# Kernel tuning notes

Measured on AMD Instinct MI355X. Metric: run time of the kernel, lower is better.

The kernel has to match this reference:

```python
import jax, jax.numpy as jnp
import numpy as np
import math

B, L, H, NH = 4, 1024, 512, 8
D = H // NH

def setup_inputs() -> dict:
    key = jax.random.key(0)
    ks = jax.random.split(key, 12)
    s = 1.0 / math.sqrt(H)
    return {
        "key": jax.random.normal(ks[0], (B, L, H), jnp.float32),
        "query": jax.random.normal(ks[1], (B, L, H), jnp.float32),
        "value": jax.random.normal(ks[2], (B, L, H), jnp.float32),
        "rel_pos_embedding": jax.random.normal(ks[3], (B, NH, L, L), jnp.float32),
        "wk_w": jax.random.normal(ks[4], (H, H), jnp.float32) * s,
        "wk_b": jnp.zeros((H,), jnp.float32),
        "wq_w": jax.random.normal(ks[5], (H, H), jnp.float32) * s,
        "wq_b": jnp.zeros((H,), jnp.float32),
        "wv_w": jax.random.normal(ks[6], (H, H), jnp.float32) * s,
        "wv_b": jnp.zeros((H,), jnp.float32),
        "ff_w": jax.random.normal(ks[7], (H, H), jnp.float32) * s,
        "ff_b": jnp.zeros((H,), jnp.float32),
        "seq_len": jax.random.randint(ks[8], (B,), 1, 768, jnp.int32),
        "lex_num": jax.random.randint(ks[9], (B,), 0, 256, jnp.int32),
    }

def reference(key, query, value, rel_pos_embedding, wk_w, wk_b, wq_w, wq_b, wv_w, wv_b, ff_w, ff_b, seq_len, lex_num):
    b, l, h = key.shape
    # projections (torch Linear: x @ W^T + b)
    k = (key @ wk_w.T + wk_b).reshape(b, l, NH, D)
    q = (query @ wq_w.T + wq_b).reshape(b, l, NH, D)
    v = (value @ wv_w.T + wv_b).reshape(b, l, NH, D)
    # QK^T: [b, nh, lq, lk]
    scores = jnp.einsum("bqhd,bkhd->bhqk", q, k) / math.sqrt(D)
    scores = scores + rel_pos_embedding
    # padding mask over key positions
    lengths = (seq_len + lex_num).astype(jnp.int32)  # [b]
    mask = jnp.arange(l, dtype=jnp.int32)[None, :] < lengths[:, None]  # [b, l]
    scores = jnp.where(mask[:, None, None, :], scores, jnp.float32(-1e15))
    attn = jax.nn.softmax(scores, axis=-1)
    out = jnp.einsum("bhqk,bkhd->bqhd", attn, v).reshape(b, l, h)
    out = out @ ff_w.T + ff_b
    return out
```

## Files before the change

### kernel.cpp

```cpp
#include <hip/hip_runtime.h>
#include <hip/hip_bf16.h>

typedef __attribute__((ext_vector_type(8))) short bf16x8;
typedef __attribute__((ext_vector_type(4))) float f32x4;

__device__ __forceinline__ unsigned short f2bf(float f) {
    return __builtin_bit_cast(unsigned short, __float2bfloat16(f));
}

typedef const __attribute__((address_space(1))) void gvoid;
typedef __attribute__((address_space(3))) void lvoid;
#define GLDS(g, s) __builtin_amdgcn_global_load_lds((gvoid*)(g), (lvoid*)(s), 16, 0, 0)

__device__ __forceinline__ void block_barrier() {
    asm volatile("" ::: "memory");
    __builtin_amdgcn_s_barrier();
    asm volatile("" ::: "memory");
}

__global__ __launch_bounds__(256) void proj_kernel(
    const float* __restrict__ query, const float* __restrict__ key_, const float* __restrict__ value,
    const float* __restrict__ wq_w, const float* __restrict__ wq_b,
    const float* __restrict__ wk_w, const float* __restrict__ wk_b,
    const float* __restrict__ wv_w, const float* __restrict__ wv_b,
    unsigned short* __restrict__ Qb, unsigned short* __restrict__ Kb, unsigned short* __restrict__ Vt)
{
    const int wid = (blockIdx.x & 7) * 48 + (blockIdx.x >> 3);
    const int z = wid >> 7;
    const int rr = wid & 127;
    const int by = rr >> 2, bx = rr & 3;

    const float* X    = (z == 0) ? query : (z == 1) ? key_ : value;
    const float* W    = (z == 0) ? wq_w  : (z == 1) ? wk_w : wv_w;
    const float* bias = (z == 0) ? wq_b  : (z == 1) ? wk_b : wv_b;

    const int t = threadIdx.x;
    const int l = t & 63;
    const int w = t >> 6;
    const int wm = w >> 1, wn = w & 1;
    const int m0 = by * 128, n0 = bx * 128;

    __shared__ __align__(16) unsigned short As[128 * 32];
    __shared__ __align__(16) unsigned short Bs[128 * 32];

    f32x4 acc[4][4];
#pragma unroll
    for (int i = 0; i < 4; i++)
#pragma unroll
        for (int j = 0; j < 4; j++) acc[i][j] = (f32x4){0.f, 0.f, 0.f, 0.f};

    float4 ra[4], rb[4];
    auto LOAD = [&](int k0) {
#pragma unroll
        for (int i = 0; i < 4; i++) {
            int idx = t + 256 * i;
            int row = idx >> 3, c = idx & 7;
            ra[i] = *(const float4*)(X + (size_t)(m0 + row) * 512 + k0 + c * 4);
            rb[i] = *(const float4*)(W + (size_t)(n0 + row) * 512 + k0 + c * 4);
        }
    };
    LOAD(0);

    for (int k0 = 0; k0 < 512; k0 += 32) {
        if (k0) block_barrier();
#pragma unroll
        for (int i = 0; i < 4; i++) {
            int idx = t + 256 * i;
            int row = idx >> 3, c = idx & 7;
            __align__(8) unsigned short va[4] = {f2bf(ra[i].x), f2bf(ra[i].y), f2bf(ra[i].z), f2bf(ra[i].w)};
            *(uint2*)(As + row * 32 + (((c >> 1) ^ (row & 3)) * 8) + (c & 1) * 4) = *(uint2*)va;
            __align__(8) unsigned short vb[4] = {f2bf(rb[i].x), f2bf(rb[i].y), f2bf(rb[i].z), f2bf(rb[i].w)};
            *(uint2*)(Bs + row * 32 + (((c >> 1) ^ (row & 3)) * 8) + (c & 1) * 4) = *(uint2*)vb;
        }
        asm volatile("s_waitcnt lgkmcnt(0)" ::: "memory");
        block_barrier();
        if (k0 + 32 < 512) LOAD(k0 + 32);

        bf16x8 af[4], bfv[4];
#pragma unroll
        for (int mf = 0; mf < 4; mf++) {
            int row = wm * 64 + mf * 16 + (l & 15);
            af[mf] = *(const bf16x8*)(As + row * 32 + (((l >> 4) ^ (row & 3)) * 8));
        }
#pragma unroll
        for (int nf = 0; nf < 4; nf++) {
            int row = wn * 64 + nf * 16 + (l & 15);
            bfv[nf] = *(const bf16x8*)(Bs + row * 32 + (((l >> 4) ^ (row & 3)) * 8));
        }
#pragma unroll
        for (int mf = 0; mf < 4; mf++)
#pragma unroll
            for (int nf = 0; nf < 4; nf++)
                acc[mf][nf] = __builtin_amdgcn_mfma_f32_16x16x32_bf16(af[mf], bfv[nf], acc[mf][nf], 0, 0, 0);
    }

    if (z < 2) {
        unsigned short* dst = (z == 0) ? Qb : Kb;
#pragma unroll
        for (int nf = 0; nf < 4; nf++) {
            int n = n0 + wn * 64 + nf * 16 + (l & 15);
            float bv = bias[n];
            int h = n >> 6, d = n & 63;
#pragma unroll
            for (int mf = 0; mf < 4; mf++) {
                int mbase = m0 + wm * 64 + mf * 16 + 4 * (l >> 4);
                int bb = mbase >> 10;
#pragma unroll
                for (int r = 0; r < 4; r++) {
                    int lq = (mbase + r) & 1023;
                    dst[((size_t)(bb * 8 + h) * 1024 + lq) * 64 + d] = f2bf(acc[mf][nf][r] + bv);
                }
            }
        }
    } else {
#pragma unroll
        for (int nf = 0; nf < 4; nf++) {
            int n = n0 + wn * 64 + nf * 16 + (l & 15);
            float bv = bias[n];
            int h = n >> 6, d = n & 63;
#pragma unroll
            for (int mf = 0; mf < 4; mf++) {
                int mbase = m0 + wm * 64 + mf * 16 + 4 * (l >> 4);
                int bb = mbase >> 10;
                int lq0 = mbase & 1023;
                ushort4 pk;
                pk.x = f2bf(acc[mf][nf][0] + bv);
                pk.y = f2bf(acc[mf][nf][1] + bv);
                pk.z = f2bf(acc[mf][nf][2] + bv);
                pk.w = f2bf(acc[mf][nf][3] + bv);
                *(ushort4*)(Vt + ((size_t)(bb * 8 + h) * 64 + d) * 1024 + lq0) = pk;
            }
        }
    }
}

__global__ __launch_bounds__(256, 3) void attn_kernel(
    const unsigned short* __restrict__ Qb, const unsigned short* __restrict__ Kb,
    const unsigned short* __restrict__ Vt, const float* __restrict__ rel_pos,
    const int* __restrict__ seq_len, const int* __restrict__ lex_num,
    unsigned short* __restrict__ AO)
{
    const int t = threadIdx.x;
    const int l = t & 63;
    const int w = t >> 6;
    const int wid = (blockIdx.x & 7) * 64 + (blockIdx.x >> 3);
    const int x8 = wid >> 6;
    const int g  = (wid >> 4) & 3;
    const int qt = wid & 15;
    const int b  = g;
    const int h  = (x8 + 2 * g) & 7;
    const int q0 = qt * 64;
    const int bh = b * 8 + h;
    const int len = seq_len[b] + lex_num[b];
    const int nkt = (len + 63) >> 6;

    __shared__ __align__(16) unsigned short Qs[64 * 64];
    __shared__ __align__(16) unsigned short Ks[2][64 * 64];
    __shared__ __align__(16) unsigned short Vs[2][64 * 64];
    __shared__ __align__(16) unsigned short Ps[4 * 16 * 64];

    const unsigned short* Qg = Qb + ((size_t)bh * 1024 + q0) * 64;
    const unsigned short* Kg = Kb + (size_t)bh * 1024 * 64;
    const unsigned short* Vg = Vt + (size_t)bh * 64 * 1024;
    const float* Rg = rel_pos + ((size_t)bh * 1024 + q0) * 1024;

    const int rl8 = l >> 3, c8 = l & 7;
    const int kvc = (c8 ^ rl8) * 8;

    auto STAGE_KV = [&](int kt2, int nb) {
        const int k0s = kt2 * 64;
#pragma unroll
        for (int j = 0; j < 2; j++) {
            int row = w * 16 + j * 8 + rl8;
            GLDS(Kg + (size_t)(k0s + row) * 64 + kvc, &Ks[nb][(w * 16 + j * 8) * 64]);
            GLDS(Vg + (size_t)row * 1024 + k0s + kvc, &Vs[nb][(w * 16 + j * 8) * 64]);
        }
    };
    auto RELLOAD = [&](float (&R)[16], int kt2) {
        const float* rp = Rg + (size_t)(w * 16 + 4 * (l >> 4)) * 1024 + kt2 * 64 + (l & 15);
#pragma unroll
        for (int r = 0; r < 4; r++)
#pragma unroll
            for (int kn = 0; kn < 4; kn++)
                R[4 * r + kn] = rp[(size_t)r * 1024 + kn * 16];
    };

    float rA[16], rB[16];
#pragma unroll
    for (int j = 0; j < 2; j++) {
        int row = w * 16 + j * 8 + rl8;
        GLDS(Qg + (size_t)row * 64 + kvc, &Qs[(w * 16 + j * 8) * 64]);
    }
    STAGE_KV(0, 0);
    RELLOAD(rA, 0);

    bf16x8 qf[2];
    f32x4 oacc[4];
#pragma unroll
    for (int dn = 0; dn < 4; dn++) oacc[dn] = (f32x4){0.f, 0.f, 0.f, 0.f};
    float m_run[4] = {-3.0e38f, -3.0e38f, -3.0e38f, -3.0e38f};
    float l_run[4] = {0.f, 0.f, 0.f, 0.f};
    unsigned short* Pw = Ps + w * 1024;

    auto tile_body = [&](int kt, float (&REL)[16], float (&RELN)[16]) {
        const int cur = kt & 1;
        const int k0 = kt * 64;
        if (kt + 1 < nkt) {
            STAGE_KV(kt + 1, cur ^ 1);
            RELLOAD(RELN, kt + 1);
            asm volatile("s_waitcnt vmcnt(20)" ::: "memory");
        } else {
            asm volatile("s_waitcnt vmcnt(0)" ::: "memory");
        }
        block_barrier();

        if (kt == 0) {
#pragma unroll
            for (int s = 0; s < 2; s++) {
                int row = w * 16 + (l & 15);
                int ch = 4 * s + (l >> 4);
                qf[s] = *(const bf16x8*)(Qs + row * 64 + ((ch ^ (row & 7)) * 8));
            }
        }

        const unsigned short* Ksc = Ks[cur];
        const unsigned short* Vsc = Vs[cur];

        f32x4 sa[4];
#pragma unroll
        for (int kn = 0; kn < 4; kn++) sa[kn] = (f32x4){0.f, 0.f, 0.f, 0.f};
        __builtin_amdgcn_s_setprio(1);
#pragma unroll
        for (int s = 0; s < 2; s++)
#pragma unroll
            for (int kn = 0; kn < 4; kn++) {
                int krow = kn * 16 + (l & 15);
                int ch = 4 * s + (l >> 4);
                bf16x8 kf = *(const bf16x8*)(Ksc + krow * 64 + ((ch ^ (krow & 7)) * 8));
                sa[kn] = __builtin_amdgcn_mfma_f32_16x16x32_bf16(qf[s], kf, sa[kn], 0, 0, 0);
            }
        __builtin_amdgcn_s_setprio(0);

        float p[4][4];
#pragma unroll
        for (int r = 0; r < 4; r++) {
            float sv[4];
#pragma unroll
            for (int kn = 0; kn < 4; kn++) {
                int kg = k0 + kn * 16 + (l & 15);
                float x = sa[kn][r] * 0.125f + REL[4 * r + kn];
                sv[kn] = (kg < len) ? x : -1e15f;
            }
            float mx = fmaxf(fmaxf(sv[0], sv[1]), fmaxf(sv[2], sv[3]));
#pragma unroll
            for (int o = 1; o < 16; o <<= 1) mx = fmaxf(mx, __shfl_xor(mx, o, 64));
            float mn = fmaxf(m_run[r], mx);
            float scale = __expf(m_run[r] - mn);
            m_run[r] = mn;
            float rs = 0.f;
#pragma unroll
            for (int kn = 0; kn < 4; kn++) { p[kn][r] = __expf(sv[kn] - mn); rs += p[kn][r]; }
#pragma unroll
            for (int o = 1; o < 16; o <<= 1) rs += __shfl_xor(rs, o, 64);
            l_run[r] = l_run[r] * scale + rs;
#pragma unroll
            for (int dn = 0; dn < 4; dn++) oacc[dn][r] *= scale;
        }

#pragma unroll
        for (int kn = 0; kn < 4; kn++)
#pragma unroll
            for (int r = 0; r < 4; r++) {
                int qrow = 4 * (l >> 4) + r;
                int k = kn * 16 + (l & 15);
                Pw[qrow * 64 + (((k >> 3) ^ (qrow & 7)) * 8) + (k & 7)] = f2bf(p[kn][r]);
            }

        __builtin_amdgcn_s_setprio(1);
#pragma unroll
        for (int s = 0; s < 2; s++) {
            int arow = (l & 15);
            bf16x8 pf = *(const bf16x8*)(Pw + arow * 64 + (((4 * s + (l >> 4)) ^ (arow & 7)) * 8));
#pragma unroll
            for (int dn = 0; dn < 4; dn++) {
                int drow = dn * 16 + (l & 15);
                bf16x8 vf = *(const bf16x8*)(Vsc + drow * 64 + (((4 * s + (l >> 4)) ^ (drow & 7)) * 8));
                oacc[dn] = __builtin_amdgcn_mfma_f32_16x16x32_bf16(pf, vf, oacc[dn], 0, 0, 0);
            }
        }
        __builtin_amdgcn_s_setprio(0);
        block_barrier();
    };

    for (int kt = 0; kt < nkt; kt += 2) {
        tile_body(kt, rA, rB);
        if (kt + 1 < nkt) tile_body(kt + 1, rB, rA);
    }

    unsigned short* AOg = AO + ((size_t)(b * 1024 + q0 + w * 16)) * 512 + h * 64;
#pragma unroll
    for (int r = 0; r < 4; r++) {
        float inv = 1.0f / l_run[r];
        int qrow = 4 * (l >> 4) + r;
#pragma unroll
        for (int dn = 0; dn < 4; dn++)
            AOg[(size_t)qrow * 512 + dn * 16 + (l & 15)] = f2bf(oacc[dn][r] * inv);
    }
}

__global__ __launch_bounds__(256) void ff_kernel(
    const unsigned short* __restrict__ AO, const float* __restrict__ ff_w,
    const float* __restrict__ ff_b, float* __restrict__ out)
{
    const int t = threadIdx.x;
    const int l = t & 63;
    const int w = t >> 6;
    const int wm = w >> 1, wn = w & 1;
    const int wid = (blockIdx.x & 7) * 32 + (blockIdx.x >> 3);
    const int by = wid >> 2;
    const int bx = wid & 3;
    const int m0 = by * 64, n0 = bx * 128;

    __shared__ __align__(16) unsigned short As[64 * 32];
    __shared__ __align__(16) unsigned short Bs[128 * 32];

    f32x4 acc[2][4];
#pragma unroll
    for (int i = 0; i < 2; i++)
#pragma unroll
        for (int j = 0; j < 4; j++) acc[i][j] = (f32x4){0.f, 0.f, 0.f, 0.f};

    uint4 ua;
    float4 rbf[4];
    const int arow = t >> 2, ac = t & 3;
    auto LOAD = [&](int k0) {
        ua = *(const uint4*)(AO + (size_t)(m0 + arow) * 512 + k0 + ac * 8);
#pragma unroll
        for (int i = 0; i < 4; i++) {
            int idx = t + 256 * i;
            int row = idx >> 3, c = idx & 7;
            rbf[i] = *(const float4*)(ff_w + (size_t)(n0 + row) * 512 + k0 + c * 4);
        }
    };
    LOAD(0);

    for (int k0 = 0; k0 < 512; k0 += 32) {
        if (k0) block_barrier();
        *(uint4*)(As + arow * 32 + ((ac ^ (arow & 3)) * 8)) = ua;
#pragma unroll
        for (int i = 0; i < 4; i++) {
            int idx = t + 256 * i;
            int row = idx >> 3, c = idx & 7;
            __align__(8) unsigned short vb[4] = {f2bf(rbf[i].x), f2bf(rbf[i].y), f2bf(rbf[i].z), f2bf(rbf[i].w)};
            *(uint2*)(Bs + row * 32 + (((c >> 1) ^ (row & 3)) * 8) + (c & 1) * 4) = *(uint2*)vb;
        }
        asm volatile("s_waitcnt lgkmcnt(0)" ::: "memory");
        block_barrier();
        if (k0 + 32 < 512) LOAD(k0 + 32);

        bf16x8 af[2], bfv[4];
#pragma unroll
        for (int mf = 0; mf < 2; mf++) {
            int row = wm * 32 + mf * 16 + (l & 15);
            af[mf] = *(const bf16x8*)(As + row * 32 + (((l >> 4) ^ (row & 3)) * 8));
        }
#pragma unroll
        for (int nf = 0; nf < 4; nf++) {
            int row = wn * 64 + nf * 16 + (l & 15);
            bfv[nf] = *(const bf16x8*)(Bs + row * 32 + (((l >> 4) ^ (row & 3)) * 8));
        }
#pragma unroll
        for (int mf = 0; mf < 2; mf++)
#pragma unroll
            for (int nf = 0; nf < 4; nf++)
                acc[mf][nf] = __builtin_amdgcn_mfma_f32_16x16x32_bf16(af[mf], bfv[nf], acc[mf][nf], 0, 0, 0);
    }

#pragma unroll
    for (int nf = 0; nf < 4; nf++) {
        int n = n0 + wn * 64 + nf * 16 + (l & 15);
        float bv = ff_b[n];
#pragma unroll
        for (int mf = 0; mf < 2; mf++) {
            int mbase = m0 + wm * 32 + mf * 16 + 4 * (l >> 4);
#pragma unroll
            for (int r = 0; r < 4; r++)
                out[(size_t)(mbase + r) * 512 + n] = acc[mf][nf][r] + bv;
        }
    }
}

extern "C" void kernel_launch(void* const* d_in, const int* in_sizes, int n_in,
                              void* d_out, int out_size, void* d_ws, size_t ws_size,
                              hipStream_t stream) {
    const float* key   = (const float*)d_in[0];
    const float* query = (const float*)d_in[1];
    const float* value = (const float*)d_in[2];
    const float* rel   = (const float*)d_in[3];
    const float* wk_w  = (const float*)d_in[4];
    const float* wk_b  = (const float*)d_in[5];
    const float* wq_w  = (const float*)d_in[6];
    const float* wq_b  = (const float*)d_in[7];
    const float* wv_w  = (const float*)d_in[8];
    const float* wv_b  = (const float*)d_in[9];
    const float* ff_w  = (const float*)d_in[10];
    const float* ff_b  = (const float*)d_in[11];
    const int* seq_len = (const int*)d_in[12];
    const int* lex_num = (const int*)d_in[13];
    float* out = (float*)d_out;

    unsigned short* Qb = (unsigned short*)d_ws;
    unsigned short* Kb = Qb + 2097152;
    unsigned short* Vt = Kb + 2097152;
    unsigned short* AO = Vt + 2097152;

    proj_kernel<<<dim3(384), 256, 0, stream>>>(query, key, value,
                                               wq_w, wq_b, wk_w, wk_b, wv_w, wv_b,
                                               Qb, Kb, Vt);
    attn_kernel<<<dim3(512), 256, 0, stream>>>(Qb, Kb, Vt, rel, seq_len, lex_num, AO);
    ff_kernel<<<dim3(256), 256, 0, stream>>>(AO, ff_w, ff_b, out);
}
```

Baseline: 69.96 us.

## Widen attention KV tile to 128 keys with single-buffered V and split staging

```diff
diff --git a/kernel.cpp b/kernel.cpp
--- a/kernel.cpp
+++ b/kernel.cpp
@@ -134,7 +134,7 @@
     }
 }
 
-__global__ __launch_bounds__(256, 3) void attn_kernel(
+__global__ __launch_bounds__(256, 2) void attn_kernel(
     const unsigned short* __restrict__ Qb, const unsigned short* __restrict__ Kb,
     const unsigned short* __restrict__ Vt, const float* __restrict__ rel_pos,
     const int* __restrict__ seq_len, const int* __restrict__ lex_num,
@@ -152,12 +152,12 @@
     const int q0 = qt * 64;
     const int bh = b * 8 + h;
     const int len = seq_len[b] + lex_num[b];
-    const int nkt = (len + 63) >> 6;
+    const int nkt = (len + 127) >> 7;
 
     __shared__ __align__(16) unsigned short Qs[64 * 64];
-    __shared__ __align__(16) unsigned short Ks[2][64 * 64];
-    __shared__ __align__(16) unsigned short Vs[2][64 * 64];
-    __shared__ __align__(16) unsigned short Ps[4 * 16 * 64];
+    __shared__ __align__(16) unsigned short Ks[2][128 * 64];
+    __shared__ __align__(16) unsigned short Vs[64 * 128];
+    __shared__ __align__(16) unsigned short Ps[4 * 16 * 128];
 
     const unsigned short* Qg = Qb + ((size_t)bh * 1024 + q0) * 64;
     const unsigned short* Kg = Kb + (size_t)bh * 1024 * 64;
@@ -166,33 +166,43 @@
 
     const int rl8 = l >> 3, c8 = l & 7;
     const int kvc = (c8 ^ rl8) * 8;
-
-    auto STAGE_KV = [&](int kt2, int nb) {
-        const int k0s = kt2 * 64;
-#pragma unroll
-        for (int j = 0; j < 2; j++) {
-            int row = w * 16 + j * 8 + rl8;
-            GLDS(Kg + (size_t)(k0s + row) * 64 + kvc, &Ks[nb][(w * 16 + j * 8) * 64]);
-            GLDS(Vg + (size_t)row * 1024 + k0s + kvc, &Vs[nb][(w * 16 + j * 8) * 64]);
-        }
-    };
-    auto RELLOAD = [&](float (&R)[16], int kt2) {
-        const float* rp = Rg + (size_t)(w * 16 + 4 * (l >> 4)) * 1024 + kt2 * 64 + (l & 15);
+    const int rl4 = l >> 4, c16 = l & 15;
+
+    auto STAGE_K = [&](int kt2, int nb) {
+        const int k0s = kt2 * 128;
+#pragma unroll
+        for (int j = 0; j < 4; j++) {
+            int row = j * 32 + w * 8 + rl8;
+            GLDS(Kg + (size_t)(k0s + row) * 64 + kvc, &Ks[nb][(j * 32 + w * 8) * 64]);
+        }
+    };
+    auto STAGE_V = [&](int kt2) {
+        const int k0s = kt2 * 128;
+#pragma unroll
+        for (int j = 0; j < 4; j++) {
+            int drow = j * 16 + w * 4 + rl4;
+            int sc = (c16 ^ (w * 4 + rl4)) * 8;
+            GLDS(Vg + (size_t)drow * 1024 + k0s + sc, &Vs[(j * 16 + w * 4) * 128]);
+        }
+    };
+    auto RELLOAD = [&](float (&R)[32], int kt2) {
+        const float* rp = Rg + (size_t)(w * 16 + 4 * (l >> 4)) * 1024 + kt2 * 128 + (l & 15);
 #pragma unroll
         for (int r = 0; r < 4; r++)
 #pragma unroll
-            for (int kn = 0; kn < 4; kn++)
-                R[4 * r + kn] = rp[(size_t)r * 1024 + kn * 16];
-    };
-
-    float rA[16], rB[16];
+            for (int kn = 0; kn < 8; kn++)
+                R[r * 8 + kn] = rp[(size_t)r * 1024 + kn * 16];
+    };
+
+    float rA[32], rB[32];
 #pragma unroll
     for (int j = 0; j < 2; j++) {
         int row = w * 16 + j * 8 + rl8;
         GLDS(Qg + (size_t)row * 64 + kvc, &Qs[(w * 16 + j * 8) * 64]);
     }
-    STAGE_KV(0, 0);
+    STAGE_K(0, 0);
     RELLOAD(rA, 0);
+    STAGE_V(0);
 
     bf16x8 qf[2];
     f32x4 oacc[4];
@@ -200,17 +210,17 @@
     for (int dn = 0; dn < 4; dn++) oacc[dn] = (f32x4){0.f, 0.f, 0.f, 0.f};
     float m_run[4] = {-3.0e38f, -3.0e38f, -3.0e38f, -3.0e38f};
     float l_run[4] = {0.f, 0.f, 0.f, 0.f};
-    unsigned short* Pw = Ps + w * 1024;
-
-    auto tile_body = [&](int kt, float (&REL)[16], float (&RELN)[16]) {
+    unsigned short* Pw = Ps + w * 16 * 128;
+
+    auto tile_body = [&](int kt, float (&REL)[32], float (&RELN)[32]) {
         const int cur = kt & 1;
-        const int k0 = kt * 64;
+        const int k0 = kt * 128;
         if (kt + 1 < nkt) {
-            STAGE_KV(kt + 1, cur ^ 1);
+            STAGE_K(kt + 1, cur ^ 1);
             RELLOAD(RELN, kt + 1);
-            asm volatile("s_waitcnt vmcnt(20)" ::: "memory");
+            asm volatile("s_waitcnt vmcnt(40)" ::: "memory");
         } else {
-            asm volatile("s_waitcnt vmcnt(0)" ::: "memory");
+            asm volatile("s_waitcnt vmcnt(4)" ::: "memory");
         }
         block_barrier();
 
@@ -224,16 +234,15 @@
         }
 
         const unsigned short* Ksc = Ks[cur];
-        const unsigned short* Vsc = Vs[cur];
-
-        f32x4 sa[4];
-#pragma unroll
-        for (int kn = 0; kn < 4; kn++) sa[kn] = (f32x4){0.f, 0.f, 0.f, 0.f};
+
+        f32x4 sa[8];
+#pragma unroll
+        for (int kn = 0; kn < 8; kn++) sa[kn] = (f32x4){0.f, 0.f, 0.f, 0.f};
         __builtin_amdgcn_s_setprio(1);
 #pragma unroll
         for (int s = 0; s < 2; s++)
 #pragma unroll
-            for (int kn = 0; kn < 4; kn++) {
+            for (int kn = 0; kn < 8; kn++) {
                 int krow = kn * 16 + (l & 15);
                 int ch = 4 * s + (l >> 4);
                 bf16x8 kf = *(const bf16x8*)(Ksc + krow * 64 + ((ch ^ (krow & 7)) * 8));
@@ -241,55 +250,60 @@
             }
         __builtin_amdgcn_s_setprio(0);
 
-        float p[4][4];
 #pragma unroll
         for (int r = 0; r < 4; r++) {
-            float sv[4];
-#pragma unroll
-            for (int kn = 0; kn < 4; kn++) {
+            float sv[8];
+#pragma unroll
+            for (int kn = 0; kn < 8; kn++) {
                 int kg = k0 + kn * 16 + (l & 15);
-                float x = sa[kn][r] * 0.125f + REL[4 * r + kn];
+                float x = sa[kn][r] * 0.125f + REL[r * 8 + kn];
                 sv[kn] = (kg < len) ? x : -1e15f;
             }
-            float mx = fmaxf(fmaxf(sv[0], sv[1]), fmaxf(sv[2], sv[3]));
+            float mx = fmaxf(fmaxf(fmaxf(sv[0], sv[1]), fmaxf(sv[2], sv[3])),
+                             fmaxf(fmaxf(sv[4], sv[5]), fmaxf(sv[6], sv[7])));
 #pragma unroll
             for (int o = 1; o < 16; o <<= 1) mx = fmaxf(mx, __shfl_xor(mx, o, 64));
             float mn = fmaxf(m_run[r], mx);
             float scale = __expf(m_run[r] - mn);
             m_run[r] = mn;
-            float rs = 0.f;
-#pragma unroll
-            for (int kn = 0; kn < 4; kn++) { p[kn][r] = __expf(sv[kn] - mn); rs += p[kn][r]; }
+            float p[8], rs = 0.f;
+#pragma unroll
+            for (int kn = 0; kn < 8; kn++) { p[kn] = __expf(sv[kn] - mn); rs += p[kn]; }
 #pragma unroll
             for (int o = 1; o < 16; o <<= 1) rs += __shfl_xor(rs, o, 64);
             l_run[r] = l_run[r] * scale + rs;
 #pragma unroll
             for (int dn = 0; dn < 4; dn++) oacc[dn][r] *= scale;
-        }
-
-#pragma unroll
-        for (int kn = 0; kn < 4; kn++)
-#pragma unroll
-            for (int r = 0; r < 4; r++) {
-                int qrow = 4 * (l >> 4) + r;
-                int k = kn * 16 + (l & 15);
-                Pw[qrow * 64 + (((k >> 3) ^ (qrow & 7)) * 8) + (k & 7)] = f2bf(p[kn][r]);
-            }
+            int qrow = 4 * (l >> 4) + r;
+#pragma unroll
+            for (int kn = 0; kn < 8; kn++) {
+                int ck = (kn * 2 + ((l >> 3) & 1)) ^ (qrow & 15);
+                Pw[qrow * 128 + ck * 8 + (l & 7)] = f2bf(p[kn]);
+            }
+        }
+
+        if (kt + 1 < nkt) {
+            asm volatile("s_waitcnt vmcnt(36)" ::: "memory");
+        } else {
+            asm volatile("s_waitcnt vmcnt(0)" ::: "memory");
+        }
+        block_barrier();
 
         __builtin_amdgcn_s_setprio(1);
 #pragma unroll
-        for (int s = 0; s < 2; s++) {
+        for (int s = 0; s < 4; s++) {
             int arow = (l & 15);
-            bf16x8 pf = *(const bf16x8*)(Pw + arow * 64 + (((4 * s + (l >> 4)) ^ (arow & 7)) * 8));
+            bf16x8 pf = *(const bf16x8*)(Pw + arow * 128 + (((s * 4 + (l >> 4)) ^ arow) * 8));
 #pragma unroll
             for (int dn = 0; dn < 4; dn++) {
                 int drow = dn * 16 + (l & 15);
-                bf16x8 vf = *(const bf16x8*)(Vsc + drow * 64 + (((4 * s + (l >> 4)) ^ (drow & 7)) * 8));
+                bf16x8 vf = *(const bf16x8*)(Vs + drow * 128 + (((s * 4 + (l >> 4)) ^ (drow & 15)) * 8));
                 oacc[dn] = __builtin_amdgcn_mfma_f32_16x16x32_bf16(pf, vf, oacc[dn], 0, 0, 0);
             }
         }
         __builtin_amdgcn_s_setprio(0);
         block_barrier();
+        if (kt + 1 < nkt) STAGE_V(kt + 1);
     };
 
     for (int kt = 0; kt < nkt; kt += 2) {
```

Result: faster. 62.87 us (-10.1%).
